# Kernel optimization log

Hardware: AMD Instinct MI355X
Metric: run time of the kernel (lower is better)

## Reference

```python
import jax, jax.numpy as jnp
import numpy as np

# ---- Config constants (from DGM Config) ----
DIM = 20        # number of assets; inputs have DIM+1 cols (last is time)
DELTA = 0.01    # finite-difference step / covariance scale
RHO = 0.5       # asset correlation
MC = 32         # Config.mc_num
N = 2048        # interior points (inputs holds 2*N rows)
UNITS = 128     # Config.unit_num
LAYERS = 3      # Config.layer_num
SIG = 0.2       # Config._sig
MU = 0.05       # Config._mu
R = 0.05        # Config._r

_cov = DELTA * (np.full((DIM, DIM), RHO, dtype=np.float64) + (1.0 - RHO) * np.eye(DIM))
L_TRIL = jnp.asarray(np.linalg.cholesky(_cov).astype(np.float32))  # (DIM, DIM) lower-tri


def setup_inputs() -> dict:
    key = jax.random.key(0)
    ks = jax.random.split(key, 20)
    d = DIM + 1
    u = lambda k, shp: jax.random.uniform(k, shp, jnp.float32, -0.05, 0.05)
    inp = {
        # strictly positive inputs so boundary prod**(1/DIM) is well-defined
        "inputs": jax.random.uniform(ks[0], (2 * N, d), jnp.float32, 0.1, 1.0),
        "eps": jax.random.normal(ks[1], (MC, N, DIM), jnp.float32),
        "w1": u(ks[2], (d, UNITS)), "b1": u(ks[3], (UNITS,)),
        "uzl": u(ks[4], (d, UNITS)), "wzl": u(ks[5], (UNITS, UNITS)), "bzl": u(ks[6], (UNITS,)),
        "ugl": u(ks[7], (d, UNITS)), "wgl": u(ks[8], (UNITS, UNITS)), "bgl": u(ks[9], (UNITS,)),
        "url": u(ks[10], (d, UNITS)), "wrl": u(ks[11], (UNITS, UNITS)), "brl": u(ks[12], (UNITS,)),
        "uhl": u(ks[13], (d, UNITS)), "whl": u(ks[14], (UNITS, UNITS)), "bhl": u(ks[15], (UNITS,)),
        "w": u(ks[16], (UNITS, 1)), "b": u(ks[17], (1,)),
    }
    return inp


def _value(x, w1, b1, uzl, wzl, bzl, ugl, wgl, bgl, url, wrl, brl, uhl, whl, bhl, w, b):
    # DGM gated residual network; x: (..., DIM+1) -> (..., 1)
    act = jnp.tanh
    s = act(x @ w1 + b1)
    for _ in range(LAYERS):
        z = act(x @ uzl + s @ wzl + bzl)
        g = act(x @ ugl + s @ wgl + bgl)
        r = act(x @ url + s @ wrl + brl)
        h = act(x @ uhl + (s * r) @ whl + bhl)
        s = (1.0 - g) * h + z * s
    return s @ w + b


def reference(inputs, eps, w1, b1, uzl, wzl, bzl, ugl, wgl, bgl, url, wrl, brl,
              uhl, whl, bhl, w, b):
    params = (w1, b1, uzl, wzl, bzl, ugl, wgl, bgl, url, wrl, brl, uhl, whl, bhl, w, b)
    val = lambda x: _value(x, *params)
    x1, x2 = jnp.split(inputs, 2, axis=0)          # interior / boundary points

    # first-order grad of value w.r.t. interior inputs
    fprime = jax.grad(lambda x: val(x).sum())(x1)  # (N, DIM+1)
    drift = jnp.concatenate([MU * x1[:, :-1], jnp.ones((x1.shape[0], 1), x1.dtype)], axis=1)
    term1_1 = jnp.sum(drift * fprime, axis=1)      # (N,)

    # correlated MVN perturbations (reparameterized): loc + eps @ L^T
    loc = x1[:, :-1]                               # (N, DIM)
    sample = loc[None, :, :] + jnp.einsum('mnd,kd->mnk', eps, L_TRIL)  # (MC, N, DIM)
    xdiff = sample * (SIG * loc)[None, :, :]
    violation = jnp.concatenate([xdiff, jnp.zeros((MC, x1.shape[0], 1), x1.dtype)], axis=2)
    xplus = x1[None, :, :] + violation             # (MC, N, DIM+1)

    fprime_plus = jax.grad(lambda x: val(x).sum())(xplus)  # (MC, N, DIM+1)
    term1_2 = jnp.sum(
        jnp.mean((fprime_plus - fprime[None, :, :]) / DELTA * violation, axis=0), axis=1)

    # boundary residual: value - payoff (geometric-mean call payoff)
    payoff = jax.nn.relu(jnp.power(jnp.prod(x2[:, :-1], axis=1), 1.0 / DIM))
    term2 = jnp.squeeze(val(x2), -1) - payoff

    interior = term1_1 + 0.5 * term1_2 - R * jnp.squeeze(val(x1), -1)
    return jnp.concatenate([interior, term2], axis=0)  # (2N,)
```

## Files before the change

kernel.cpp:

```cpp
#include <hip/hip_runtime.h>
#include <math.h>

#define DIMN 20
#define DD 21
#define NN 2048
#define MCN 32
#define UNITS 128
#define SIGC 0.2f
#define MUC 0.05f
#define RC 0.05f
#define DELTAC 0.01f

#define TM 32
#define KCH 24
#define KC3 8
#define PTOT (NN + MCN*NN + NN)
#define NBLK (PTOT/TM)

#define OFF_L 0
#define OFF_WT 512
#define OFF_UZGR (OFF_WT + 4*16384)
#define OFF_WZGR (OFF_UZGR + 8192)
#define OFF_FP1  (OFF_WZGR + 49152)
#define OFF_VAL1 (OFF_FP1 + NN*DD)
#define OFF_VAL2 (OFF_VAL1 + NN)
#define OFF_T12  (OFF_VAL2 + NN)
#define OFF_GATES (OFF_T12 + NN)

#define ST_S1 0
#define ST_Z1 4096
#define ST_G1 8192
#define ST_R1 12288
#define ST_Z2 16384
#define ST_G2 20480
#define ST_R2 24576
#define GB_STRIDE 28672

#define L_TOT_SG 19776
#define L_TOT_RC 23872

#define ELT44(...) _Pragma("unroll") for (int p = 0; p < 4; p++){ _Pragma("unroll") for (int jj = 0; jj < 4; jj++){ __VA_ARGS__; } }

__device__ __forceinline__ int offq(int row, int p0){
    return row*32 + ((p0 + 4*(row&7)) & 31);
}
__device__ __forceinline__ int offs(int row, int p){
    return row*32 + (((p & 28) + 4*(row&7)) & 31) + (p & 3);
}

__device__ __forceinline__ float ftanh(float x){
    float cx = fminf(9.f, fmaxf(-9.f, x));
    float e  = __expf(2.f*cx);
    return fmaf(-2.f, __builtin_amdgcn_rcpf(e + 1.f), 1.f);
}

__device__ __forceinline__ void stageW(const float* __restrict__ g, float* wc, int units){
#if defined(__has_builtin) && __has_builtin(__builtin_amdgcn_global_load_lds)
    int lane = threadIdx.x & 63, wid = threadIdx.x >> 6;
    for (int base = wid*64; base < units; base += 256){
        int u = base + lane;
        if (u < units)
            __builtin_amdgcn_global_load_lds(
                (const __attribute__((address_space(1))) unsigned int*)(g) + (size_t)u*4,
                (__attribute__((address_space(3))) unsigned int*)(wc) + (size_t)base*4,
                16, 0, 0);
    }
#else
    int t = threadIdx.x;
    for (int u = t; u < units; u += 256){
        float4 v = *(const float4*)(g + u*4);
        *(float4*)(wc + u*4) = v;
    }
#endif
}

#define FMA16(acc, s4, w4) \
  acc[0][0]=fmaf(s4.x,w4.x,acc[0][0]); acc[0][1]=fmaf(s4.x,w4.y,acc[0][1]); \
  acc[0][2]=fmaf(s4.x,w4.z,acc[0][2]); acc[0][3]=fmaf(s4.x,w4.w,acc[0][3]); \
  acc[1][0]=fmaf(s4.y,w4.x,acc[1][0]); acc[1][1]=fmaf(s4.y,w4.y,acc[1][1]); \
  acc[1][2]=fmaf(s4.y,w4.z,acc[1][2]); acc[1][3]=fmaf(s4.y,w4.w,acc[1][3]); \
  acc[2][0]=fmaf(s4.z,w4.x,acc[2][0]); acc[2][1]=fmaf(s4.z,w4.y,acc[2][1]); \
  acc[2][2]=fmaf(s4.z,w4.z,acc[2][2]); acc[2][3]=fmaf(s4.z,w4.w,acc[2][3]); \
  acc[3][0]=fmaf(s4.w,w4.x,acc[3][0]); acc[3][1]=fmaf(s4.w,w4.y,acc[3][1]); \
  acc[3][2]=fmaf(s4.w,w4.z,acc[3][2]); acc[3][3]=fmaf(s4.w,w4.w,acc[3][3]);

__device__ __forceinline__ void mmU_d(const float* __restrict__ gU, int K,
    const float* __restrict__ vec, float acc[4][4], int jg, int p0)
{
    const float* up = gU + 4*jg;
    #pragma unroll 4
    for (int k = 0; k < K; k++){
        float4 w4 = *(const float4*)(up + k*UNITS);
        float4 s4 = *(const float4*)(vec + offq(k, p0));
        FMA16(acc, s4, w4)
    }
}
__device__ __forceinline__ void mmU3_d(const float* __restrict__ gU, int K,
    const float* __restrict__ vec, float a0[4][4], float a1[4][4], float a2[4][4],
    int jg, int p0)
{
    const float* up = gU + 4*jg;
    #pragma unroll 2
    for (int k = 0; k < K; k++){
        const float* r = up + k*384;
        float4 s4 = *(const float4*)(vec + offq(k, p0));
        float4 w0 = *(const float4*)(r);
        float4 w1v = *(const float4*)(r + 128);
        float4 w2 = *(const float4*)(r + 256);
        FMA16(a0, s4, w0) FMA16(a1, s4, w1v) FMA16(a2, s4, w2)
    }
}

__device__ __forceinline__ void mm_acc(const float* __restrict__ gW, int K,
    const float* __restrict__ vec, float acc[4][4], float* __restrict__ Wc,
    int jg, int p0)
{
    int nch = (K + KCH - 1) / KCH;
    {
        int r0 = (K < KCH) ? K : KCH;
        stageW(gW, Wc, r0*32);
    }
    for (int c = 0; c < nch; c++){
        __syncthreads();
        if (c + 1 < nch){
            int c0n = (c+1)*KCH;
            int rn = K - c0n; if (rn > KCH) rn = KCH;
            stageW(gW + c0n*UNITS, Wc + ((c+1)&1)*KCH*UNITS, rn*32);
        }
        int c0 = c*KCH;
        int rows = K - c0; if (rows > KCH) rows = KCH;
        const float* wb = Wc + (c&1)*KCH*UNITS;
        if (rows == KCH){
            #pragma unroll 4
            for (int kk = 0; kk < KCH; kk++){
                int k = c0 + kk;
                float4 w4 = *(const float4*)(wb + kk*UNITS + 4*jg);
                float4 s4 = *(const float4*)(vec + offq(k, p0));
                FMA16(acc, s4, w4)
            }
        } else {
            for (int kk = 0; kk < rows; kk++){
                int k = c0 + kk;
                float4 w4 = *(const float4*)(wb + kk*UNITS + 4*jg);
                float4 s4 = *(const float4*)(vec + offq(k, p0));
                FMA16(acc, s4, w4)
            }
        }
    }
    __syncthreads();
}

__device__ __forceinline__ void mm3_acc(const float* __restrict__ gW, int K,
    const float* __restrict__ vec, float az[4][4], float ag[4][4], float ar[4][4],
    float* __restrict__ Wc, int jg, int p0)
{
    int nch = (K + KC3 - 1) / KC3;
    {
        int r0 = (K < KC3) ? K : KC3;
        stageW(gW, Wc, r0*96);
    }
    for (int c = 0; c < nch; c++){
        __syncthreads();
        if (c + 1 < nch){
            int c0n = (c+1)*KC3;
            int rn = K - c0n; if (rn > KC3) rn = KC3;
            stageW(gW + c0n*384, Wc + ((c+1)&1)*(KC3*384), rn*96);
        }
        int c0 = c*KC3;
        int rows = K - c0; if (rows > KC3) rows = KC3;
        const float* wb = Wc + (c&1)*(KC3*384);
        if (rows == KC3){
            #pragma unroll 2
            for (int kk = 0; kk < KC3; kk++){
                int k = c0 + kk;
                const float* wrow = wb + kk*384 + 4*jg;
                float4 s4  = *(const float4*)(vec + offq(k, p0));
                float4 wz4 = *(const float4*)(wrow);
                float4 wg4 = *(const float4*)(wrow + 128);
                float4 wr4 = *(const float4*)(wrow + 256);
                FMA16(az, s4, wz4)
                FMA16(ag, s4, wg4)
                FMA16(ar, s4, wr4)
            }
        } else {
            for (int kk = 0; kk < rows; kk++){
                int k = c0 + kk;
                const float* wrow = wb + kk*384 + 4*jg;
                float4 s4  = *(const float4*)(vec + offq(k, p0));
                float4 wz4 = *(const float4*)(wrow);
                float4 wg4 = *(const float4*)(wrow + 128);
                float4 wr4 = *(const float4*)(wrow + 256);
                FMA16(az, s4, wz4)
                FMA16(ag, s4, wg4)
                FMA16(ar, s4, wr4)
            }
        }
    }
    __syncthreads();
}

__device__ __forceinline__ void write_own(float* buf, const float v[4][4], int j0, int p0){
    #pragma unroll
    for (int jj = 0; jj < 4; jj++){
        int j = j0 + jj;
        float4 q = make_float4(v[0][jj], v[1][jj], v[2][jj], v[3][jj]);
        *(float4*)(buf + offq(j, p0)) = q;
    }
}
__device__ __forceinline__ void read_own(const float* buf, float v[4][4], int j0, int p0){
    #pragma unroll
    for (int jj = 0; jj < 4; jj++){
        int j = j0 + jj;
        float4 q = *(const float4*)(buf + offq(j, p0));
        v[0][jj]=q.x; v[1][jj]=q.y; v[2][jj]=q.z; v[3][jj]=q.w;
    }
}
__device__ __forceinline__ void stash_w(float* buf, const float v[4][4], int t){
    #pragma unroll
    for (int jj = 0; jj < 4; jj++)
        *(float4*)(buf + (jj*256 + t)*4) = make_float4(v[0][jj], v[1][jj], v[2][jj], v[3][jj]);
}
__device__ __forceinline__ void stash_r(const float* buf, float v[4][4], int t){
    #pragma unroll
    for (int jj = 0; jj < 4; jj++){
        float4 q = *(const float4*)(buf + (jj*256 + t)*4);
        v[0][jj]=q.x; v[1][jj]=q.y; v[2][jj]=q.z; v[3][jj]=q.w;
    }
}

__device__ __forceinline__ void gate_f(const float* __restrict__ U, const float* __restrict__ W,
    const float* __restrict__ bias, const float* __restrict__ xT, const float* __restrict__ Sin,
    float* __restrict__ Wc, float out[4][4], int jg, int p0, int j0)
{
    float acc[4][4];
    float4 b = *(const float4*)(bias + j0);
    #pragma unroll
    for (int p = 0; p < 4; p++){ acc[p][0]=b.x; acc[p][1]=b.y; acc[p][2]=b.z; acc[p][3]=b.w; }
    mmU_d(U, DD, xT, acc, jg, p0);
    mm_acc(W, UNITS, Sin, acc, Wc, jg, p0);
    #pragma unroll
    for (int p = 0; p < 4; p++)
        #pragma unroll
        for (int jj = 0; jj < 4; jj++) out[p][jj] = ftanh(acc[p][jj]);
}

__device__ __forceinline__ void gate3_f(const float* __restrict__ Uzgr, const float* __restrict__ Wzgr,
    const float* __restrict__ bz, const float* __restrict__ bg, const float* __restrict__ br,
    const float* __restrict__ xT, const float* __restrict__ Sin,
    float* __restrict__ Wc, float zt[4][4], float gt[4][4], float rt[4][4],
    int jg, int p0, int j0)
{
    float4 b0 = *(const float4*)(bz + j0);
    float4 b1 = *(const float4*)(bg + j0);
    float4 b2 = *(const float4*)(br + j0);
    #pragma unroll
    for (int p = 0; p < 4; p++){
        zt[p][0]=b0.x; zt[p][1]=b0.y; zt[p][2]=b0.z; zt[p][3]=b0.w;
        gt[p][0]=b1.x; gt[p][1]=b1.y; gt[p][2]=b1.z; gt[p][3]=b1.w;
        rt[p][0]=b2.x; rt[p][1]=b2.y; rt[p][2]=b2.z; rt[p][3]=b2.w;
    }
    mmU3_d(Uzgr, DD, xT, zt, gt, rt, jg, p0);
    mm3_acc(Wzgr, UNITS, Sin, zt, gt, rt, Wc, jg, p0);
    ELT44(zt[p][jj]=ftanh(zt[p][jj]); gt[p][jj]=ftanh(gt[p][jj]); rt[p][jj]=ftanh(rt[p][jj]))
}

__global__ void chol_kernel(float* __restrict__ Lout)
{
    if (threadIdx.x == 0 && blockIdx.x == 0) {
        const double beta = 0.01 * 0.5;
        const double diag = 0.01;
        double c[DIMN], d[DIMN];
        double S = 0.0;
        for (int j = 0; j < DIMN; j++){
            double dj = sqrt(diag - S);
            double cj = (beta - S) / dj;
            d[j] = dj; c[j] = cj;
            S += cj*cj;
        }
        for (int i = 0; i < DIMN; i++)
            for (int j = 0; j < DIMN; j++)
                Lout[i*DIMN + j] = (j < i) ? (float)c[j] : (j == i) ? (float)d[i] : 0.0f;
    }
}

__global__ void transpose_k(const float* __restrict__ wz, const float* __restrict__ wg,
                            const float* __restrict__ wr, const float* __restrict__ wh,
                            float* __restrict__ WT)
{
    int idx = blockIdx.x*256 + threadIdx.x;
    int q = idx >> 14, r2 = idx & 16383, k = r2 >> 7, j = r2 & 127;
    const float* src = (q==0)? wz : (q==1)? wg : (q==2)? wr : wh;
    WT[(q<<14) + j*UNITS + k] = src[k*UNITS + j];
}

__global__ void pack_zgr(const float* __restrict__ uz, const float* __restrict__ ug,
                         const float* __restrict__ ur,
                         const float* __restrict__ wz, const float* __restrict__ wg,
                         const float* __restrict__ wr,
                         float* __restrict__ Uzgr, float* __restrict__ Wzgr)
{
    int idx = blockIdx.x*256 + threadIdx.x;
    if (idx < 128*384){
        int k = idx/384, c = idx - k*384, g = c >> 7, j = c & 127;
        const float* s = (g==0)? wz : (g==1)? wg : wr;
        Wzgr[idx] = s[k*UNITS + j];
        return;
    }
    int i2 = idx - 128*384;
    if (i2 < 21*384){
        int k = i2/384, c = i2 - k*384, g = c >> 7, j = c & 127;
        const float* s = (g==0)? uz : (g==1)? ug : ur;
        Uzgr[i2] = s[k*UNITS + j];
    }
}

#define DGM_PARAMS \
    const float* __restrict__ inputs, const float* __restrict__ eps, \
    const float* __restrict__ w1, const float* __restrict__ b1, \
    const float* __restrict__ uz, const float* __restrict__ bz, \
    const float* __restrict__ ug, const float* __restrict__ bg, \
    const float* __restrict__ ur, const float* __restrict__ br, \
    const float* __restrict__ uh, const float* __restrict__ wh, const float* __restrict__ bh, \
    const float* __restrict__ wv, const float* __restrict__ bv, \
    const float* __restrict__ Lm, const float* __restrict__ WT, \
    const float* __restrict__ Uzgr, const float* __restrict__ Wzgr, \
    float* __restrict__ gws, \
    float* __restrict__ fp1, float* __restrict__ val1, float* __restrict__ val2, \
    float* __restrict__ t12acc

#define DGM_ARGS inputs, eps, w1, b1, uz, bz, ug, bg, ur, br, uh, wh, bh, wv, bv, \
    Lm, WT, Uzgr, Wzgr, gws, fp1, val1, val2, t12acc

template<int SG>
__device__ __forceinline__ void dgm_body(float* lds, DGM_PARAMS)
{
    float* S0 = lds;
    float* S1 = SG ? lds : lds + 4096;
    float* S2 = lds + (SG ? 4096 : 8192);
    float* Db = lds + (SG ? 8192 : 12288);
    float* Wc = lds + (SG ? 12288 : 16384);
    float* xT = lds + (SG ? 18432 : 22528);
    float* Vb = lds + (SG ? 19104 : 23200);

    const int t  = threadIdx.x;
    const int jg = t & 31;
    const int pg = t >> 5;
    const int p0 = pg * 4;
    const int j0 = jg * 4;
    const int P0 = blockIdx.x * TM;
    const int type = (P0 < NN) ? 0 : (P0 < NN + MCN*NN) ? 1 : 2;
    int base_n = 0, mrow = 0;
    if (type == 1){ int q = P0 - NN; mrow = q >> 11; base_n = q & (NN-1); }

    float* gb = gws + (size_t)blockIdx.x * GB_STRIDE;

    {
        int p = t & 31, kq = t >> 5;
        for (int ki = 0; ki < 3; ki++){
            int k = kq + 8*ki;
            if (k > DIMN) break;
            float xv;
            if (type == 0){
                xv = inputs[(P0 + p)*DD + k];
            } else if (type == 2){
                xv = inputs[(NN + (P0 - NN - MCN*NN) + p)*DD + k];
            } else {
                int n = base_n + p;
                float x1v = inputs[n*DD + k];
                if (k == DIMN) xv = x1v;
                else {
                    const float* ep = eps + (size_t)(mrow*NN + n)*DIMN;
                    float a = x1v;
                    for (int d = 0; d < DIMN; d++) a = fmaf(ep[d], Lm[k*DIMN + d], a);
                    float viol = a * (SIGC * x1v);
                    Vb[offs(k, p)] = viol;
                    xv = x1v + viol;
                }
            }
            xT[offs(k, p)] = xv;
        }
    }
    __syncthreads();

    float s_own[4][4];
    {
        float acc[4][4];
        float4 b = *(const float4*)(b1 + j0);
        #pragma unroll
        for (int p = 0; p < 4; p++){ acc[p][0]=b.x; acc[p][1]=b.y; acc[p][2]=b.z; acc[p][3]=b.w; }
        mmU_d(w1, DD, xT, acc, jg, p0);
        ELT44(s_own[p][jj] = ftanh(acc[p][jj]))
        write_own(S0, s_own, j0, p0);
        __syncthreads();
    }

    float zt[4][4], gt[4][4], rt[4][4], ht[4][4];

#define GATES(SIN, SMUL) \
    gate3_f(Uzgr, Wzgr, bz, bg, br, xT, SIN, Wc, zt, gt, rt, jg, p0, j0); \
    { float tt[4][4]; ELT44(tt[p][jj] = SMUL[p][jj]*rt[p][jj]) write_own(Db, tt, j0, p0); } \
    gate_f(uh, wh, bh, xT, Db, Wc, ht, jg, p0, j0);

#define FWD_LAYER(SIN) \
    GATES(SIN, s_own) \
    ELT44(s_own[p][jj] = (1.f - gt[p][jj])*ht[p][jj] + zt[p][jj]*s_own[p][jj])

    FWD_LAYER(S0)
    if (SG){ if (type != 2){
        stash_w(gb + ST_S1, s_own, t);
        stash_w(gb + ST_Z1, zt, t); stash_w(gb + ST_G1, gt, t); stash_w(gb + ST_R1, rt, t);
    } }
    else   { write_own(S1, s_own, j0, p0); }
    write_own(Db, s_own, j0, p0);

    FWD_LAYER(Db)
    if (SG && type != 2){
        stash_w(gb + ST_Z2, zt, t); stash_w(gb + ST_G2, gt, t); stash_w(gb + ST_R2, rt, t);
    }
    write_own(S2, s_own, j0, p0);

    FWD_LAYER(S2)

    {
        float4 wv4 = *(const float4*)(wv + j0);
        float vs[4];
        #pragma unroll
        for (int p = 0; p < 4; p++)
            vs[p] = s_own[p][0]*wv4.x + s_own[p][1]*wv4.y + s_own[p][2]*wv4.z + s_own[p][3]*wv4.w;
        __syncthreads();
        *(float4*)(Db + jg*32 + p0) = make_float4(vs[0], vs[1], vs[2], vs[3]);
        __syncthreads();
        if (t < TM){
            float v = bv[0];
            for (int j2 = 0; j2 < 32; j2++) v += Db[j2*32 + t];
            if (type == 0) val1[P0 + t] = v;
            else if (type == 2) val2[P0 + t - NN - MCN*NN] = v;
        }
        __syncthreads();
    }
    if (type == 2) return;

    float ds[4][4];
    {
        float4 wv4 = *(const float4*)(wv + j0);
        #pragma unroll
        for (int p = 0; p < 4; p++){ ds[p][0]=wv4.x; ds[p][1]=wv4.y; ds[p][2]=wv4.z; ds[p][3]=wv4.w; }
    }
    float proj[4] = {0.f, 0.f, 0.f, 0.f};
    float dxp[3] = {0.f, 0.f, 0.f};
    const int pi = t >> 3, il = t & 7;

    const float* WTz = WT;
    const float* WTg = WT + 16384;
    const float* WTr = WT + 2*16384;
    const float* WTh = WT + 3*16384;

#define DX_DOT(UMAT) \
    { _Pragma("unroll") for (int ii = 0; ii < 3; ii++){ \
        int i = il + 8*ii; \
        if (i < DD){ \
            const float* Urow = UMAT + i*UNITS; \
            float a = 0.f; \
            for (int j2 = 0; j2 < UNITS; j2++) a = fmaf(Db[offs(j2, pi)], Urow[j2], a); \
            dxp[ii] += a; \
        } } }

#define PROJ_D(UMAT, SEL) \
    { float uv[4][4]; \
      ELT44(uv[p][jj] = 0.f) \
      mmU_d(UMAT, DIMN, Vb, uv, jg, p0); \
      ELT44(proj[p] += uv[p][jj]*SEL[p][jj]) }

#define BWD_LAYER(SLP, MODE, GZ, GG, GR) \
    { \
    float dsn[4][4]; \
    if (MODE == 1){ \
        float slg[4][4]; read_own(SLP, slg, j0, p0); \
        GATES(SLP, slg) \
    } \
    {  \
        float sl[4][4], zv[4][4]; \
        if (MODE == 2){ stash_r(gb + ST_S1, sl, t); stash_r(gb + GZ, zv, t); } \
        else if (MODE == 3){ read_own(SLP, sl, j0, p0); stash_r(gb + GZ, zv, t); } \
        else if (MODE == 0){ read_own(S2, sl, j0, p0); ELT44(zv[p][jj] = zt[p][jj]) } \
        else { read_own(SLP, sl, j0, p0); ELT44(zv[p][jj] = zt[p][jj]) } \
        float dzp[4][4]; \
        ELT44(float d=ds[p][jj]; float zz=zv[p][jj]; \
            dzp[p][jj] = d*sl[p][jj]*(1.f - zz*zz); dsn[p][jj] = d*zz) \
        write_own(Db, dzp, j0, p0); \
        if (type == 1){ PROJ_D(uz, dzp) } else { __syncthreads(); DX_DOT(uz) } \
    } \
    mm_acc(WTz, UNITS, Db, dsn, Wc, jg, p0); \
    float dhp[4][4]; \
    {  \
        float gv[4][4], hv[4][4]; \
        if (MODE == 2 || MODE == 3){ \
            float zv[4][4], sl[4][4], sn[4][4]; \
            stash_r(gb + GZ, zv, t); stash_r(gb + GG, gv, t); \
            if (MODE == 2){ stash_r(gb + ST_S1, sl, t); read_own(S2, sn, j0, p0); } \
            else { read_own(SLP, sl, j0, p0); stash_r(gb + ST_S1, sn, t); } \
            ELT44(hv[p][jj] = (sn[p][jj] - zv[p][jj]*sl[p][jj]) / (1.f - gv[p][jj])) \
        } else { ELT44(gv[p][jj] = gt[p][jj]; hv[p][jj] = ht[p][jj]) } \
        float dgp[4][4]; \
        ELT44(float d=ds[p][jj]; float gg=gv[p][jj]; float hh=hv[p][jj]; \
            dgp[p][jj] = -d*hh*(1.f - gg*gg); \
            dhp[p][jj] = d*(1.f - gg)*(1.f - hh*hh)) \
        write_own(Db, dgp, j0, p0); \
        if (type == 1){ PROJ_D(ug, dgp) } else { __syncthreads(); DX_DOT(ug) } \
    } \
    mm_acc(WTg, UNITS, Db, dsn, Wc, jg, p0); \
    write_own(Db, dhp, j0, p0); \
    if (type == 1){ PROJ_D(uh, dhp) } else { __syncthreads(); DX_DOT(uh) } \
    float dsr[4][4]; \
    ELT44(dsr[p][jj] = 0.f) \
    mm_acc(WTh, UNITS, Db, dsr, Wc, jg, p0); \
    {  \
        float rv[4][4], sl[4][4], drp[4][4]; \
        if (MODE == 2){ stash_r(gb + GR, rv, t); stash_r(gb + ST_S1, sl, t); } \
        else if (MODE == 3){ stash_r(gb + GR, rv, t); read_own(SLP, sl, j0, p0); } \
        else if (MODE == 0){ ELT44(rv[p][jj] = rt[p][jj]) read_own(S2, sl, j0, p0); } \
        else { ELT44(rv[p][jj] = rt[p][jj]) read_own(SLP, sl, j0, p0); } \
        ELT44(float dr=dsr[p][jj]; float rr=rv[p][jj]; \
            drp[p][jj] = dr*sl[p][jj]*(1.f - rr*rr); dsn[p][jj] += dr*rr) \
        write_own(Db, drp, j0, p0); \
        if (type == 1){ PROJ_D(ur, drp) } else { __syncthreads(); DX_DOT(ur) } \
    } \
    mm_acc(WTr, UNITS, Db, dsn, Wc, jg, p0); \
    ELT44(ds[p][jj] = dsn[p][jj]) \
    }

    BWD_LAYER(S0, 0, ST_Z2, ST_G2, ST_R2)
    BWD_LAYER(S1, (SG ? 2 : 1), ST_Z2, ST_G2, ST_R2)
    if (SG){ BWD_LAYER(S0, 3, ST_Z1, ST_G1, ST_R1) }
    else   { BWD_LAYER(S0, 1, ST_Z1, ST_G1, ST_R1) }

    {
        float s0l[4][4];
        read_own(S0, s0l, j0, p0);
        float v0[4][4];
        ELT44(v0[p][jj] = ds[p][jj]*(1.f - s0l[p][jj]*s0l[p][jj]))

        if (type == 1){
            PROJ_D(w1, v0)
            __syncthreads();
            *(float4*)(Db + jg*32 + p0) = make_float4(proj[0], proj[1], proj[2], proj[3]);
            __syncthreads();
            if (t < TM){
                float s = 0.f;
                for (int j2 = 0; j2 < 32; j2++) s += Db[j2*32 + t];
                atomicAdd(t12acc + base_n + t, s);
            }
        } else {
            write_own(Db, v0, j0, p0);
            __syncthreads();
            DX_DOT(w1)
            #pragma unroll
            for (int ii = 0; ii < 3; ii++){
                int i = il + 8*ii;
                if (i < DD) fp1[(P0 + pi)*DD + i] = dxp[ii];
            }
        }
    }
}

__global__ __launch_bounds__(256) __attribute__((amdgpu_waves_per_eu(2,2))) void dgm_sg(DGM_PARAMS){
    __shared__ float lds[L_TOT_SG];
    dgm_body<1>(lds, DGM_ARGS);
}
__global__ __launch_bounds__(256) __attribute__((amdgpu_waves_per_eu(2,2))) void dgm_rc(DGM_PARAMS){
    __shared__ float lds[L_TOT_RC];
    dgm_body<0>(lds, DGM_ARGS);
}

__global__ void finalize_k(const float* __restrict__ inputs, const float* __restrict__ eps,
    const float* __restrict__ Lm, const float* __restrict__ fp1, const float* __restrict__ val1,
    const float* __restrict__ val2, const float* __restrict__ t12acc, float* __restrict__ out)
{
    int n = blockIdx.x*256 + threadIdx.x;
    if (n >= NN) return;
    float fp[DD];
    #pragma unroll
    for (int k = 0; k < DD; k++) fp[k] = fp1[n*DD + k];
    float t11 = fp[DIMN];
    #pragma unroll
    for (int k = 0; k < DIMN; k++) t11 = fmaf(MUC*inputs[n*DD + k], fp[k], t11);
    float esum[DIMN];
    #pragma unroll
    for (int d = 0; d < DIMN; d++){
        float a = 0.f;
        for (int m = 0; m < MCN; m++) a += eps[(size_t)(m*NN + n)*DIMN + d];
        esum[d] = a;
    }
    float t12b = 0.f;
    #pragma unroll
    for (int k = 0; k < DIMN; k++){
        float loc = inputs[n*DD + k];
        float ssum = (float)MCN * loc;
        #pragma unroll
        for (int d = 0; d < DIMN; d++) ssum = fmaf(esum[d], Lm[k*DIMN + d], ssum);
        float vsum = ssum * (SIGC*loc);
        t12b = fmaf(fp[k], vsum, t12b);
    }
    float term12 = (t12acc[n] - t12b) * (1.0f/(DELTAC*(float)MCN));
    out[n] = t11 + 0.5f*term12 - RC*val1[n];

    float prod = 1.f;
    #pragma unroll
    for (int k = 0; k < DIMN; k++) prod *= inputs[(NN + n)*DD + k];
    float payoff = powf(prod, 1.0f/(float)DIMN);
    if (!(payoff > 0.f)) payoff = 0.f;
    out[NN + n] = val2[n] - payoff;
}

extern "C" void kernel_launch(void* const* d_in, const int* in_sizes, int n_in,
                              void* d_out, int out_size, void* d_ws, size_t ws_size,
                              hipStream_t stream)
{
    const float* inputs = (const float*)d_in[0];
    const float* eps    = (const float*)d_in[1];
    const float* w1     = (const float*)d_in[2];
    const float* b1     = (const float*)d_in[3];
    const float* uz     = (const float*)d_in[4];
    const float* wz     = (const float*)d_in[5];
    const float* bz     = (const float*)d_in[6];
    const float* ug     = (const float*)d_in[7];
    const float* wg     = (const float*)d_in[8];
    const float* bg     = (const float*)d_in[9];
    const float* urr    = (const float*)d_in[10];
    const float* wr     = (const float*)d_in[11];
    const float* br     = (const float*)d_in[12];
    const float* uh     = (const float*)d_in[13];
    const float* wh     = (const float*)d_in[14];
    const float* bh     = (const float*)d_in[15];
    const float* wv     = (const float*)d_in[16];
    const float* bv     = (const float*)d_in[17];

    float* ws    = (float*)d_ws;
    float* Lm    = ws + OFF_L;
    float* WT    = ws + OFF_WT;
    float* Uzgr  = ws + OFF_UZGR;
    float* Wzgr  = ws + OFF_WZGR;
    float* fp1   = ws + OFF_FP1;
    float* val1  = ws + OFF_VAL1;
    float* val2  = ws + OFF_VAL2;
    float* t12   = ws + OFF_T12;
    float* gates = ws + OFF_GATES;
    float* out   = (float*)d_out;

    hipMemsetAsync(t12, 0, NN*sizeof(float), stream);
    hipLaunchKernelGGL(chol_kernel, dim3(1), dim3(64), 0, stream, Lm);
    hipLaunchKernelGGL(transpose_k, dim3(256), dim3(256), 0, stream, wz, wg, wr, wh, WT);
    hipLaunchKernelGGL(pack_zgr, dim3(224), dim3(256), 0, stream, uz, ug, urr, wz, wg, wr, Uzgr, Wzgr);

    size_t need_bytes = ((size_t)OFF_GATES + (size_t)NBLK * (size_t)GB_STRIDE) * sizeof(float);
    if (ws_size >= need_bytes){
        hipLaunchKernelGGL(dgm_sg, dim3(NBLK), dim3(256), 0, stream,
            inputs, eps, w1, b1, uz, bz, ug, bg, urr, br, uh, wh, bh, wv, bv,
            Lm, WT, Uzgr, Wzgr, gates, fp1, val1, val2, t12);
    } else {
        hipLaunchKernelGGL(dgm_rc, dim3(NBLK), dim3(256), 0, stream,
            inputs, eps, w1, b1, uz, bz, ug, bg, urr, br, uh, wh, bh, wv, bv,
            Lm, WT, Uzgr, Wzgr, gates, fp1, val1, val2, t12);
    }
    hipLaunchKernelGGL(finalize_k, dim3(8), dim3(256), 0, stream,
        inputs, eps, Lm, fp1, val1, val2, t12, out);
}
```

Before: 1.306 ms.

## Read hidden-weight matrices directly from global memory instead of LDS staging

Removes the double-buffered LDS staging of the 128x128 and fused 128x384 weight matrices (global_load_lds chunks) and reads the weight float4s directly from global memory/cache inside the matmul loops. This drops the per-chunk __syncthreads and staging traffic and shrinks LDS per block, but explicit barriers are added around Db writes to replace the synchronisation that mm_acc used to provide. Every thread now issues global loads for weights, which relies on L1/L2 hit rates rather than shared LDS reuse.

```diff
diff --git a/kernel.cpp b/kernel.cpp
--- a/kernel.cpp
+++ b/kernel.cpp
@@ -12,8 +12,6 @@
 #define DELTAC 0.01f
 
 #define TM 32
-#define KCH 24
-#define KC3 8
 #define PTOT (NN + MCN*NN + NN)
 #define NBLK (PTOT/TM)
 
@@ -36,8 +34,8 @@
 #define ST_R2 24576
 #define GB_STRIDE 28672
 
-#define L_TOT_SG 19776
-#define L_TOT_RC 23872
+#define L_TOT_SG 13632
+#define L_TOT_RC 17728
 
 #define ELT44(...) _Pragma("unroll") for (int p = 0; p < 4; p++){ _Pragma("unroll") for (int jj = 0; jj < 4; jj++){ __VA_ARGS__; } }
 
@@ -52,26 +50,6 @@
     float cx = fminf(9.f, fmaxf(-9.f, x));
     float e  = __expf(2.f*cx);
     return fmaf(-2.f, __builtin_amdgcn_rcpf(e + 1.f), 1.f);
-}
-
-__device__ __forceinline__ void stageW(const float* __restrict__ g, float* wc, int units){
-#if defined(__has_builtin) && __has_builtin(__builtin_amdgcn_global_load_lds)
-    int lane = threadIdx.x & 63, wid = threadIdx.x >> 6;
-    for (int base = wid*64; base < units; base += 256){
-        int u = base + lane;
-        if (u < units)
-            __builtin_amdgcn_global_load_lds(
-                (const __attribute__((address_space(1))) unsigned int*)(g) + (size_t)u*4,
-                (__attribute__((address_space(3))) unsigned int*)(wc) + (size_t)base*4,
-                16, 0, 0);
-    }
-#else
-    int t = threadIdx.x;
-    for (int u = t; u < units; u += 256){
-        float4 v = *(const float4*)(g + u*4);
-        *(float4*)(wc + u*4) = v;
-    }
-#endif
 }
 
 #define FMA16(acc, s4, w4) \
@@ -84,25 +62,25 @@
   acc[3][0]=fmaf(s4.w,w4.x,acc[3][0]); acc[3][1]=fmaf(s4.w,w4.y,acc[3][1]); \
   acc[3][2]=fmaf(s4.w,w4.z,acc[3][2]); acc[3][3]=fmaf(s4.w,w4.w,acc[3][3]);
 
-__device__ __forceinline__ void mmU_d(const float* __restrict__ gU, int K,
+__device__ __forceinline__ void mm_d(const float* __restrict__ gW, int K,
     const float* __restrict__ vec, float acc[4][4], int jg, int p0)
 {
-    const float* up = gU + 4*jg;
+    const float* wp = gW + 4*jg;
     #pragma unroll 4
     for (int k = 0; k < K; k++){
-        float4 w4 = *(const float4*)(up + k*UNITS);
+        float4 w4 = *(const float4*)(wp + k*UNITS);
         float4 s4 = *(const float4*)(vec + offq(k, p0));
         FMA16(acc, s4, w4)
     }
 }
-__device__ __forceinline__ void mmU3_d(const float* __restrict__ gU, int K,
+__device__ __forceinline__ void mm3_d(const float* __restrict__ gW, int K,
     const float* __restrict__ vec, float a0[4][4], float a1[4][4], float a2[4][4],
     int jg, int p0)
 {
-    const float* up = gU + 4*jg;
+    const float* wp = gW + 4*jg;
     #pragma unroll 2
     for (int k = 0; k < K; k++){
-        const float* r = up + k*384;
+        const float* r = wp + k*384;
         float4 s4 = *(const float4*)(vec + offq(k, p0));
         float4 w0 = *(const float4*)(r);
         float4 w1v = *(const float4*)(r + 128);
@@ -111,94 +89,6 @@
     }
 }
 
-__device__ __forceinline__ void mm_acc(const float* __restrict__ gW, int K,
-    const float* __restrict__ vec, float acc[4][4], float* __restrict__ Wc,
-    int jg, int p0)
-{
-    int nch = (K + KCH - 1) / KCH;
-    {
-        int r0 = (K < KCH) ? K : KCH;
-        stageW(gW, Wc, r0*32);
-    }
-    for (int c = 0; c < nch; c++){
-        __syncthreads();
-        if (c + 1 < nch){
-            int c0n = (c+1)*KCH;
-            int rn = K - c0n; if (rn > KCH) rn = KCH;
-            stageW(gW + c0n*UNITS, Wc + ((c+1)&1)*KCH*UNITS, rn*32);
-        }
-        int c0 = c*KCH;
-        int rows = K - c0; if (rows > KCH) rows = KCH;
-        const float* wb = Wc + (c&1)*KCH*UNITS;
-        if (rows == KCH){
-            #pragma unroll 4
-            for (int kk = 0; kk < KCH; kk++){
-                int k = c0 + kk;
-                float4 w4 = *(const float4*)(wb + kk*UNITS + 4*jg);
-                float4 s4 = *(const float4*)(vec + offq(k, p0));
-                FMA16(acc, s4, w4)
-            }
-        } else {
-            for (int kk = 0; kk < rows; kk++){
-                int k = c0 + kk;
-                float4 w4 = *(const float4*)(wb + kk*UNITS + 4*jg);
-                float4 s4 = *(const float4*)(vec + offq(k, p0));
-                FMA16(acc, s4, w4)
-            }
-        }
-    }
-    __syncthreads();
-}
-
-__device__ __forceinline__ void mm3_acc(const float* __restrict__ gW, int K,
-    const float* __restrict__ vec, float az[4][4], float ag[4][4], float ar[4][4],
-    float* __restrict__ Wc, int jg, int p0)
-{
-    int nch = (K + KC3 - 1) / KC3;
-    {
-        int r0 = (K < KC3) ? K : KC3;
-        stageW(gW, Wc, r0*96);
-    }
-    for (int c = 0; c < nch; c++){
-        __syncthreads();
-        if (c + 1 < nch){
-            int c0n = (c+1)*KC3;
-            int rn = K - c0n; if (rn > KC3) rn = KC3;
-            stageW(gW + c0n*384, Wc + ((c+1)&1)*(KC3*384), rn*96);
-        }
-        int c0 = c*KC3;
-        int rows = K - c0; if (rows > KC3) rows = KC3;
-        const float* wb = Wc + (c&1)*(KC3*384);
-        if (rows == KC3){
-            #pragma unroll 2
-            for (int kk = 0; kk < KC3; kk++){
-                int k = c0 + kk;
-                const float* wrow = wb + kk*384 + 4*jg;
-                float4 s4  = *(const float4*)(vec + offq(k, p0));
-                float4 wz4 = *(const float4*)(wrow);
-                float4 wg4 = *(const float4*)(wrow + 128);
-                float4 wr4 = *(const float4*)(wrow + 256);
-                FMA16(az, s4, wz4)
-                FMA16(ag, s4, wg4)
-                FMA16(ar, s4, wr4)
-            }
-        } else {
-            for (int kk = 0; kk < rows; kk++){
-                int k = c0 + kk;
-                const float* wrow = wb + kk*384 + 4*jg;
-                float4 s4  = *(const float4*)(vec + offq(k, p0));
-                float4 wz4 = *(const float4*)(wrow);
-                float4 wg4 = *(const float4*)(wrow + 128);
-                float4 wr4 = *(const float4*)(wrow + 256);
-                FMA16(az, s4, wz4)
-                FMA16(ag, s4, wg4)
-                FMA16(ar, s4, wr4)
-            }
-        }
-    }
-    __syncthreads();
-}
-
 __device__ __forceinline__ void write_own(float* buf, const float v[4][4], int j0, int p0){
     #pragma unroll
     for (int jj = 0; jj < 4; jj++){
@@ -230,14 +120,14 @@
 
 __device__ __forceinline__ void gate_f(const float* __restrict__ U, const float* __restrict__ W,
     const float* __restrict__ bias, const float* __restrict__ xT, const float* __restrict__ Sin,
-    float* __restrict__ Wc, float out[4][4], int jg, int p0, int j0)
+    float out[4][4], int jg, int p0, int j0)
 {
     float acc[4][4];
     float4 b = *(const float4*)(bias + j0);
     #pragma unroll
     for (int p = 0; p < 4; p++){ acc[p][0]=b.x; acc[p][1]=b.y; acc[p][2]=b.z; acc[p][3]=b.w; }
-    mmU_d(U, DD, xT, acc, jg, p0);
-    mm_acc(W, UNITS, Sin, acc, Wc, jg, p0);
+    mm_d(U, DD, xT, acc, jg, p0);
+    mm_d(W, UNITS, Sin, acc, jg, p0);
     #pragma unroll
     for (int p = 0; p < 4; p++)
         #pragma unroll
@@ -247,7 +137,7 @@
 __device__ __forceinline__ void gate3_f(const float* __restrict__ Uzgr, const float* __restrict__ Wzgr,
     const float* __restrict__ bz, const float* __restrict__ bg, const float* __restrict__ br,
     const float* __restrict__ xT, const float* __restrict__ Sin,
-    float* __restrict__ Wc, float zt[4][4], float gt[4][4], float rt[4][4],
+    float zt[4][4], float gt[4][4], float rt[4][4],
     int jg, int p0, int j0)
 {
     float4 b0 = *(const float4*)(bz + j0);
@@ -259,8 +149,8 @@
         gt[p][0]=b1.x; gt[p][1]=b1.y; gt[p][2]=b1.z; gt[p][3]=b1.w;
         rt[p][0]=b2.x; rt[p][1]=b2.y; rt[p][2]=b2.z; rt[p][3]=b2.w;
     }
-    mmU3_d(Uzgr, DD, xT, zt, gt, rt, jg, p0);
-    mm3_acc(Wzgr, UNITS, Sin, zt, gt, rt, Wc, jg, p0);
+    mm3_d(Uzgr, DD, xT, zt, gt, rt, jg, p0);
+    mm3_d(Wzgr, UNITS, Sin, zt, gt, rt, jg, p0);
     ELT44(zt[p][jj]=ftanh(zt[p][jj]); gt[p][jj]=ftanh(gt[p][jj]); rt[p][jj]=ftanh(rt[p][jj]))
 }
 
@@ -338,9 +228,8 @@
     float* S1 = SG ? lds : lds + 4096;
     float* S2 = lds + (SG ? 4096 : 8192);
     float* Db = lds + (SG ? 8192 : 12288);
-    float* Wc = lds + (SG ? 12288 : 16384);
-    float* xT = lds + (SG ? 18432 : 22528);
-    float* Vb = lds + (SG ? 19104 : 23200);
+    float* xT = lds + (SG ? 12288 : 16384);
+    float* Vb = lds + (SG ? 12960 : 17056);
 
     const int t  = threadIdx.x;
     const int jg = t & 31;
@@ -388,7 +277,7 @@
         float4 b = *(const float4*)(b1 + j0);
         #pragma unroll
         for (int p = 0; p < 4; p++){ acc[p][0]=b.x; acc[p][1]=b.y; acc[p][2]=b.z; acc[p][3]=b.w; }
-        mmU_d(w1, DD, xT, acc, jg, p0);
+        mm_d(w1, DD, xT, acc, jg, p0);
         ELT44(s_own[p][jj] = ftanh(acc[p][jj]))
         write_own(S0, s_own, j0, p0);
         __syncthreads();
@@ -397,9 +286,11 @@
     float zt[4][4], gt[4][4], rt[4][4], ht[4][4];
 
 #define GATES(SIN, SMUL) \
-    gate3_f(Uzgr, Wzgr, bz, bg, br, xT, SIN, Wc, zt, gt, rt, jg, p0, j0); \
+    gate3_f(Uzgr, Wzgr, bz, bg, br, xT, SIN, zt, gt, rt, jg, p0, j0); \
+    __syncthreads(); \
     { float tt[4][4]; ELT44(tt[p][jj] = SMUL[p][jj]*rt[p][jj]) write_own(Db, tt, j0, p0); } \
-    gate_f(uh, wh, bh, xT, Db, Wc, ht, jg, p0, j0);
+    __syncthreads(); \
+    gate_f(uh, wh, bh, xT, Db, ht, jg, p0, j0);
 
 #define FWD_LAYER(SIN) \
     GATES(SIN, s_own) \
@@ -411,13 +302,16 @@
         stash_w(gb + ST_Z1, zt, t); stash_w(gb + ST_G1, gt, t); stash_w(gb + ST_R1, rt, t);
     } }
     else   { write_own(S1, s_own, j0, p0); }
+    __syncthreads();
     write_own(Db, s_own, j0, p0);
+    __syncthreads();
 
     FWD_LAYER(Db)
     if (SG && type != 2){
         stash_w(gb + ST_Z2, zt, t); stash_w(gb + ST_G2, gt, t); stash_w(gb + ST_R2, rt, t);
     }
     write_own(S2, s_own, j0, p0);
+    __syncthreads();
 
     FWD_LAYER(S2)
 
@@ -468,7 +362,7 @@
 #define PROJ_D(UMAT, SEL) \
     { float uv[4][4]; \
       ELT44(uv[p][jj] = 0.f) \
-      mmU_d(UMAT, DIMN, Vb, uv, jg, p0); \
+      mm_d(UMAT, DIMN, Vb, uv, jg, p0); \
       ELT44(proj[p] += uv[p][jj]*SEL[p][jj]) }
 
 #define BWD_LAYER(SLP, MODE, GZ, GG, GR) \
@@ -487,10 +381,12 @@
         float dzp[4][4]; \
         ELT44(float d=ds[p][jj]; float zz=zv[p][jj]; \
             dzp[p][jj] = d*sl[p][jj]*(1.f - zz*zz); dsn[p][jj] = d*zz) \
+        __syncthreads(); \
         write_own(Db, dzp, j0, p0); \
-        if (type == 1){ PROJ_D(uz, dzp) } else { __syncthreads(); DX_DOT(uz) } \
+        __syncthreads(); \
+        if (type == 1){ PROJ_D(uz, dzp) } else { DX_DOT(uz) } \
     } \
-    mm_acc(WTz, UNITS, Db, dsn, Wc, jg, p0); \
+    mm_d(WTz, UNITS, Db, dsn, jg, p0); \
     float dhp[4][4]; \
     {  \
         float gv[4][4], hv[4][4]; \
@@ -505,15 +401,20 @@
         ELT44(float d=ds[p][jj]; float gg=gv[p][jj]; float hh=hv[p][jj]; \
             dgp[p][jj] = -d*hh*(1.f - gg*gg); \
             dhp[p][jj] = d*(1.f - gg)*(1.f - hh*hh)) \
+        __syncthreads(); \
         write_own(Db, dgp, j0, p0); \
-        if (type == 1){ PROJ_D(ug, dgp) } else { __syncthreads(); DX_DOT(ug) } \
+        __syncthreads(); \
+        if (type == 1){ PROJ_D(ug, dgp) } else { DX_DOT(ug) } \
     } \
-    mm_acc(WTg, UNITS, Db, dsn, Wc, jg, p0); \
+    mm_d(WTg, UNITS, Db, dsn, jg, p0); \
+     \
+    __syncthreads(); \
     write_own(Db, dhp, j0, p0); \
-    if (type == 1){ PROJ_D(uh, dhp) } else { __syncthreads(); DX_DOT(uh) } \
+    __syncthreads(); \
+    if (type == 1){ PROJ_D(uh, dhp) } else { DX_DOT(uh) } \
     float dsr[4][4]; \
     ELT44(dsr[p][jj] = 0.f) \
-    mm_acc(WTh, UNITS, Db, dsr, Wc, jg, p0); \
+    mm_d(WTh, UNITS, Db, dsr, jg, p0); \
     {  \
         float rv[4][4], sl[4][4], drp[4][4]; \
         if (MODE == 2){ stash_r(gb + GR, rv, t); stash_r(gb + ST_S1, sl, t); } \
@@ -522,10 +423,12 @@
         else { ELT44(rv[p][jj] = rt[p][jj]) read_own(SLP, sl, j0, p0); } \
         ELT44(float dr=dsr[p][jj]; float rr=rv[p][jj]; \
             drp[p][jj] = dr*sl[p][jj]*(1.f - rr*rr); dsn[p][jj] += dr*rr) \
+        __syncthreads(); \
         write_own(Db, drp, j0, p0); \
-        if (type == 1){ PROJ_D(ur, drp) } else { __syncthreads(); DX_DOT(ur) } \
+        __syncthreads(); \
+        if (type == 1){ PROJ_D(ur, drp) } else { DX_DOT(ur) } \
     } \
-    mm_acc(WTr, UNITS, Db, dsn, Wc, jg, p0); \
+    mm_d(WTr, UNITS, Db, dsn, jg, p0); \
     ELT44(ds[p][jj] = dsn[p][jj]) \
     }
 
@@ -551,6 +454,7 @@
                 atomicAdd(t12acc + base_n + t, s);
             }
         } else {
+            __syncthreads();
             write_own(Db, v0, j0, p0);
             __syncthreads();
             DX_DOT(w1)
```

New measurement: 1.301 ms. About the same (-0.3%).
